# Kernel optimization log

Hardware: AMD Instinct MI355X
Metric: run time of the kernel (lower is better)

## Reference

```python
import jax, jax.numpy as jnp
import numpy as np

D = 1024      # d_model
H = 16        # num_heads
HW = D // H   # head_width = 64
FF = 4 * D    # hidden_dim = 4096
BATCH = 2
T = 2048
EPS = 1e-5


def layer_norm(x, g, b):
    mu = jnp.mean(x, axis=-1, keepdims=True)
    var = jnp.mean(jnp.square(x - mu), axis=-1, keepdims=True)
    return (x - mu) * jax.lax.rsqrt(var + EPS) * g + b


def setup_inputs() -> dict:
    key = jax.random.key(0)
    ks = jax.random.split(key, 7)
    s = 0.02
    return {
        "x": jax.random.normal(ks[0], (BATCH, T, D), dtype=jnp.float32),
        "Wq": jax.random.normal(ks[1], (D, D), dtype=jnp.float32) * s,
        "Wk": jax.random.normal(ks[2], (D, D), dtype=jnp.float32) * s,
        "Wv": jax.random.normal(ks[3], (D, D), dtype=jnp.float32) * s,
        "W1": jax.random.normal(ks[4], (FF, D), dtype=jnp.float32) * s,
        "W2": jax.random.normal(ks[5], (D, FF), dtype=jnp.float32) * s,
        "g1": jnp.ones((D,), dtype=jnp.float32),
        "b1": jnp.zeros((D,), dtype=jnp.float32),
        "g2": jnp.ones((D,), dtype=jnp.float32),
        "b2": jnp.zeros((D,), dtype=jnp.float32),
    }


def reference(x, Wq, Wk, Wv, W1, W2, g1, b1, g2, b2):
    N, t, d = x.shape
    # norm1
    xn = layer_norm(x, g1, b1)

    # --- MHSA with ALiBi + causal mask (math mirrors torch module) ---
    def heads(y):  # (N,t,D) -> (N,H,t,HW)
        return y.reshape(N, t, H, HW).transpose(0, 2, 1, 3)

    q = heads(xn @ Wq.T)
    k = heads(xn @ Wk.T)
    v = heads(xn @ Wv.T)

    scores = jnp.einsum("nhqd,nhkd->nhqk", q, k) / np.sqrt(HW).astype(np.float32)

    pos = jnp.arange(t)
    rel = (pos[None, :] - pos[:, None]).astype(x.dtype)           # [t,t], rel[i,j]=j-i
    slopes = (2.0 ** (-(jnp.arange(1, H + 1)) * (8.0 / H))).astype(x.dtype)  # [H]
    alibi = slopes[:, None, None] * rel                            # [H,t,t]
    causal = jnp.where(pos[None, :] > pos[:, None],
                       jnp.array(-jnp.inf, x.dtype),
                       jnp.array(0.0, x.dtype))                    # [t,t]

    att = jax.nn.softmax(scores + alibi[None] + causal[None, None], axis=-1)
    o = jnp.einsum("nhqk,nhkd->nhqd", att, v)
    o = o.transpose(0, 2, 1, 3).reshape(N, t, d)

    att_out = xn + o

    # --- MLP: Linear -> SiLU -> Linear ---
    h = layer_norm(att_out, g2, b2)
    m = jax.nn.silu(h @ W1.T) @ W2.T
    return att_out + m
```

## Files before the change

### kernel.cpp

```cpp
#include <hip/hip_runtime.h>

#define DMODEL 1024
#define NHEAD  16
#define HWID   64
#define FFDIM  4096
#define NBATCH 2
#define SEQT   2048
#define NTOK   4096
#define QKLD   3072

using bf8    = __attribute__((ext_vector_type(8))) short;
using f32x4  = __attribute__((ext_vector_type(4))) float;
using f32x16 = __attribute__((ext_vector_type(16))) float;

__device__ inline short to_bf16(float f) {
  unsigned u = __float_as_uint(f);
  return (short)((u + 0x7fffu + ((u >> 16) & 1u)) >> 16);
}
__device__ inline float from_bf16(short s) {
  return __uint_as_float(((unsigned)(unsigned short)s) << 16);
}
__device__ inline float exp2_fast(float x) {
  float r;
  asm("v_exp_f32 %0, %1" : "=v"(r) : "v"(x));
  return r;
}
__device__ inline unsigned cvt_pk_bf16(float lo, float hi) {
  unsigned r;
  asm("v_cvt_pk_bf16_f32 %0, %1, %2" : "=v"(r) : "v"(lo), "v"(hi));
  return r;
}
__device__ inline void lds_load16(const void* g, void* l) {
  __builtin_amdgcn_global_load_lds(
      (const __attribute__((address_space(1))) void*)g,
      (__attribute__((address_space(3))) void*)l, 16, 0, 0);
}

__global__ __launch_bounds__(256)
void cvt_all(const float* __restrict__ Wq, const float* __restrict__ Wk,
             const float* __restrict__ Wv, const float* __restrict__ W1,
             const float* __restrict__ W2, short* __restrict__ wqkv,
             short* __restrict__ w1b, short* __restrict__ w2b) {
  int i = blockIdx.x * 256 + threadIdx.x;
  const float* src;
  short* dst;
  if (i < 1048576)      { src = W1; dst = w1b; }
  else if (i < 2097152) { src = W2; dst = w2b;            i -= 1048576; }
  else if (i < 2359296) { src = Wq; dst = wqkv;           i -= 2097152; }
  else if (i < 2621440) { src = Wk; dst = wqkv + 1048576; i -= 2359296; }
  else                  { src = Wv; dst = wqkv + 2097152; i -= 2621440; }
  float4 v = ((const float4*)src)[i];
  short4 o;
  o.x = to_bf16(v.x); o.y = to_bf16(v.y);
  o.z = to_bf16(v.z); o.w = to_bf16(v.w);
  ((short4*)dst)[i] = o;
}

__global__ __launch_bounds__(256)
void ln_kernel(const float* __restrict__ x, const float* __restrict__ g,
               const float* __restrict__ b, short* __restrict__ out) {
  const int row = blockIdx.x;
  const int t = threadIdx.x;
  const float4 v = ((const float4*)(x + (long)row * DMODEL))[t];
  float s  = v.x + v.y + v.z + v.w;
  float s2 = v.x * v.x + v.y * v.y + v.z * v.z + v.w * v.w;
#pragma unroll
  for (int m = 1; m < 64; m <<= 1) {
    s  += __shfl_xor(s, m);
    s2 += __shfl_xor(s2, m);
  }
  __shared__ float red[8];
  if ((t & 63) == 0) { red[t >> 6] = s; red[4 + (t >> 6)] = s2; }
  __syncthreads();
  s  = red[0] + red[1] + red[2] + red[3];
  s2 = red[4] + red[5] + red[6] + red[7];
  const float mu = s * (1.f / DMODEL);
  const float rs = rsqrtf(s2 * (1.f / DMODEL) - mu * mu + 1e-5f);
  const float4 gv = ((const float4*)g)[t];
  const float4 bv = ((const float4*)b)[t];
  short4 o;
  o.x = to_bf16((v.x - mu) * rs * gv.x + bv.x);
  o.y = to_bf16((v.y - mu) * rs * gv.y + bv.y);
  o.z = to_bf16((v.z - mu) * rs * gv.z + bv.z);
  o.w = to_bf16((v.w - mu) * rs * gv.w + bv.w);
  ((short4*)(out + (long)row * DMODEL))[t] = o;
}

template <int EPI>
__global__ __launch_bounds__(256, 3)
void gemm4(const short* __restrict__ A, const short* __restrict__ Bw,
           void* __restrict__ Cout, int N, int lda, int ldb, int Kslice) {
  __shared__ short lds[3][2][4096];
  const int tid = threadIdx.x;
  const int w = tid >> 6, lane = tid & 63;
  const int l15 = lane & 15, l4 = lane >> 4;
  const int wr = (w >> 1) * 64, wc = (w & 1) * 64;

  const int gx = gridDim.x, nwg = gx * gridDim.y;
  const int wg = blockIdx.y * gx + blockIdx.x;
  const int sw = (wg & 7) * (nwg >> 3) + (wg >> 3);
  const int sx = gx >> 2;
  const int st = sw >> 4, w16 = sw & 15;
  const long bm = (long)((st / sx) * 4 + (w16 >> 2)) * 128;
  const long bn = (long)((st % sx) * 4 + (w16 & 3)) * 128;
  const long kofs = (long)blockIdx.z * Kslice;

  long aoff[2], boff[2];
#pragma unroll
  for (int i = 0; i < 2; ++i) {
    const int c = i * 4 + w;
    const int row = c * 16 + (lane >> 2);
    const int slog = (lane & 3) ^ ((row >> 1) & 3);
    aoff[i] = (bm + row) * (long)lda + slog * 8 + kofs;
    boff[i] = (bn + row) * (long)ldb + slog * 8 + kofs;
  }
  int offA[4], offB[4];
#pragma unroll
  for (int m = 0; m < 4; ++m) {
    const int row = wr + m * 16 + l15;
    offA[m] = row * 64 + ((l4 ^ ((row >> 1) & 3)) << 4);
  }
#pragma unroll
  for (int n = 0; n < 4; ++n) {
    const int row = wc + n * 16 + l15;
    offB[n] = row * 64 + ((l4 ^ ((row >> 1) & 3)) << 4);
  }

  const int NT = Kslice >> 5;
  f32x4 acc[4][4] = {};

#pragma unroll
  for (int t = 0; t < 2; ++t) {
    char* db = (char*)&lds[t][0][0];
#pragma unroll
    for (int i = 0; i < 2; ++i) {
      const int c = i * 4 + w;
      lds_load16(A  + aoff[i] + t * 32, db + c * 1024);
      lds_load16(Bw + boff[i] + t * 32, db + 8192 + c * 1024);
    }
  }

  int slot = 0, pslot = 2;
  for (int t = 0; t < NT; ++t) {
    if (t + 1 < NT) asm volatile("s_waitcnt vmcnt(4)" ::: "memory");
    else            asm volatile("s_waitcnt vmcnt(0)" ::: "memory");
    __builtin_amdgcn_s_barrier();
    asm volatile("" ::: "memory");
    if (t + 2 < NT) {
      char* db = (char*)&lds[pslot][0][0];
      const long ks = (long)(t + 2) * 32;
#pragma unroll
      for (int i = 0; i < 2; ++i) {
        const int c = i * 4 + w;
        lds_load16(A  + aoff[i] + ks, db + c * 1024);
        lds_load16(Bw + boff[i] + ks, db + 8192 + c * 1024);
      }
    }
    const char* sb = (const char*)&lds[slot][0][0];
    bf8 af[4], bfr[4];
#pragma unroll
    for (int m = 0; m < 4; ++m) af[m] = *(const bf8*)(sb + offA[m]);
#pragma unroll
    for (int n = 0; n < 4; ++n) bfr[n] = *(const bf8*)(sb + 8192 + offB[n]);
    __builtin_amdgcn_s_setprio(1);
#pragma unroll
    for (int m = 0; m < 4; ++m)
#pragma unroll
      for (int n = 0; n < 4; ++n)
        acc[m][n] = __builtin_amdgcn_mfma_f32_16x16x32_bf16(af[m], bfr[n], acc[m][n], 0, 0, 0);
    __builtin_amdgcn_s_setprio(0);
    slot  = (slot  == 2) ? 0 : slot  + 1;
    pslot = (pslot == 2) ? 0 : pslot + 1;
  }

#pragma unroll
  for (int m = 0; m < 4; ++m)
#pragma unroll
    for (int n = 0; n < 4; ++n) {
      const long col = bn + wc + n * 16 + l15;
#pragma unroll
      for (int r = 0; r < 4; ++r) {
        const long row = bm + wr + m * 16 + l4 * 4 + r;
        float v = acc[m][n][r];
        if (EPI == 0) {
          ((short*)Cout)[row * N + col] = to_bf16(v);
        } else if (EPI == 1) {
          ((short*)Cout)[row * N + col] = to_bf16(v / (1.f + __expf(-v)));
        } else {
          atomicAdd(&((float*)Cout)[row * N + col], v);
        }
      }
    }
}

__global__ __launch_bounds__(256)
void pack_kv(const short* __restrict__ qkv, short* __restrict__ Kp,
             short* __restrict__ Vp) {
  __shared__ short tile[64][72];
  const int bx = blockIdx.x, bh = blockIdx.y;
  const int b = bh >> 4, h = bh & 15;
  const int t = threadIdx.x;
  if (bx < 64) {
    const int g = bx;
    const int row = t >> 3, cc = t & 7, c = cc >> 1, hi = cc & 1;
    const bf8 v = *(const bf8*)&qkv[(long)(b * SEQT + g * 32 + row) * QKLD +
                                    1024 + h * HWID + c * 16 + hi * 8];
    *(bf8*)&Kp[(((long)bh * 256 + g * 4 + c) * 64 + hi * 32 + row) * 8] = v;
  } else {
    const int tc = bx - 64;
    {
      const int r = t >> 2, c = (t & 3) * 16;
      const long src = (long)(b * SEQT + tc * 64 + r) * QKLD + 2048 + h * HWID + c;
      *(bf8*)&tile[r][c]     = *(const bf8*)&qkv[src];
      *(bf8*)&tile[r][c + 8] = *(const bf8*)&qkv[src + 8];
    }
    __syncthreads();
    const int dg = t >> 7, ch = (t >> 5) & 3, row = t & 31;
#pragma unroll
    for (int hi = 0; hi < 2; ++hi) {
      short o[8];
#pragma unroll
      for (int j = 0; j < 8; ++j) o[j] = tile[ch * 16 + hi * 8 + j][dg * 32 + row];
      *(bf8*)&Vp[(((long)bh * 256 + dg * 128 + tc * 4 + ch) * 64 + hi * 32 + row) * 8] =
          *(bf8*)o;
    }
  }
}

__global__ __launch_bounds__(64, 2)
void attn_kernel(const short* __restrict__ qkv, const short* __restrict__ Kp,
                 const short* __restrict__ Vp, const short* __restrict__ xn,
                 float* __restrict__ att) {
  const int L = blockIdx.x;
  const int bh = (L & 7) * 4 + ((L >> 3) & 3);
  const int qtile = 63 - (L >> 5);
  const int b = bh >> 4, h = bh & 15;
  const int q0 = qtile * 32;
  const int lane = threadIdx.x;
  const int l31 = lane & 31, hi = lane >> 5;
  const long tokbase = (long)b * SEQT;

  bf8 qf[4];
  {
    const short* qrow = qkv + (tokbase + q0 + l31) * QKLD + h * HWID + hi * 8;
#pragma unroll
    for (int c = 0; c < 4; ++c) qf[c] = *(const bf8*)(qrow + c * 16);
  }

  const float slope2 = exp2f(-0.5f * (float)(h + 1)) * 1.44269504f;
  const float sc2 = 0.125f * 1.44269504f;
  float arr[16];
#pragma unroll
  for (int r = 0; r < 16; ++r) arr[r] = slope2 * (float)((r & 3) + 8 * (r >> 2));
  const float hofs = slope2 * 4.f * (float)hi;
  const float qabs = (float)(q0 + l31);

  float m2 = -1e30f, lsum = 0.f;
  f32x16 acc0 = {}, acc1 = {};
  const int ktm = q0 >> 6;
  const bf8* kfb = (const bf8*)Kp + (long)bh * 16384 + lane;
  const bf8* vfb = (const bf8*)Vp + (long)bh * 16384 + lane;

  bf8 kc[8], kn[8], vc[8];
#pragma unroll
  for (int c = 0; c < 4; ++c) {
    kc[c]     = kfb[c * 64];
    kc[4 + c] = kfb[256 + c * 64];
  }

#pragma unroll 2
  for (int kt = 0; kt <= ktm; ++kt) {
    const int k0 = kt * 64;
    const long vb = (long)kt * 256;
#pragma unroll
    for (int ch = 0; ch < 4; ++ch) {
      vc[ch]     = vfb[vb + ch * 64];
      vc[4 + ch] = vfb[8192 + vb + ch * 64];
    }
    const long nb = (long)(kt < ktm ? kt + 1 : kt) * 512;
#pragma unroll
    for (int c = 0; c < 4; ++c) {
      kn[c]     = kfb[nb + c * 64];
      kn[4 + c] = kfb[nb + 256 + c * 64];
    }
    f32x16 s0 = {}, s1 = {};
#pragma unroll
    for (int c = 0; c < 4; ++c) {
      s0 = __builtin_amdgcn_mfma_f32_32x32x16_bf16(kc[c], qf[c], s0, 0, 0, 0);
      s1 = __builtin_amdgcn_mfma_f32_32x32x16_bf16(kc[4 + c], qf[c], s1, 0, 0, 0);
    }
    const float base = slope2 * ((float)k0 - qabs) + hofs;
    float s[32];
#pragma unroll
    for (int r = 0; r < 16; ++r) {
      s[r]      = fmaf(s0[r], sc2, base + arr[r]);
      s[16 + r] = fmaf(s1[r], sc2, base + arr[r] + slope2 * 32.f);
    }
    if (kt == ktm) {
      const int qi = q0 + l31;
#pragma unroll
      for (int r = 0; r < 16; ++r) {
        const int krel = (r & 3) + 8 * (r >> 2) + 4 * hi;
        if (k0 + krel > qi)      s[r]      = -1e30f;
        if (k0 + 32 + krel > qi) s[16 + r] = -1e30f;
      }
    }
    float ma = s[0], mb = s[1], mc = s[2], md = s[3];
#pragma unroll
    for (int i = 4; i < 32; i += 4) {
      ma = fmaxf(ma, s[i]); mb = fmaxf(mb, s[i + 1]);
      mc = fmaxf(mc, s[i + 2]); md = fmaxf(md, s[i + 3]);
    }
    float pm = fmaxf(fmaxf(ma, mb), fmaxf(mc, md));
    pm = fmaxf(pm, __shfl_xor(pm, 32));
    if (!__all(pm - m2 <= 11.0f)) {
      const float nm = fmaxf(m2, pm);
      const float alpha = exp2_fast(m2 - nm);
      m2 = nm;
      lsum *= alpha;
      acc0 *= alpha;
      acc1 *= alpha;
    }
    float p[32];
#pragma unroll
    for (int i = 0; i < 32; ++i) p[i] = exp2_fast(s[i] - m2);
    float sa = p[0], sb = p[1], sc = p[2], sd = p[3];
#pragma unroll
    for (int i = 4; i < 32; i += 4) {
      sa += p[i]; sb += p[i + 1]; sc += p[i + 2]; sd += p[i + 3];
    }
    float rs = (sa + sb) + (sc + sd);
    rs += __shfl_xor(rs, 32);
    lsum += rs;
    unsigned cpk[16];
#pragma unroll
    for (int g = 0; g < 8; ++g) {
      cpk[g]     = cvt_pk_bf16(p[2 * g], p[2 * g + 1]);
      cpk[8 + g] = cvt_pk_bf16(p[16 + 2 * g], p[16 + 2 * g + 1]);
    }
    bf8 pb[4];
#pragma unroll
    for (int ch = 0; ch < 4; ++ch) {
      const int cb = (ch >> 1) * 8 + (ch & 1) * 4;
      unsigned u0 = cpk[cb + 0], u2 = cpk[cb + 2];
      unsigned u1 = cpk[cb + 1], u3 = cpk[cb + 3];
      asm("v_permlane32_swap_b32 %0, %1" : "+v"(u0), "+v"(u2));
      asm("v_permlane32_swap_b32 %0, %1" : "+v"(u1), "+v"(u3));
      union { unsigned u[4]; bf8 v; } f;
      f.u[0] = u0; f.u[1] = u1; f.u[2] = u2; f.u[3] = u3;
      pb[ch] = f.v;
    }
#pragma unroll
    for (int ch = 0; ch < 4; ++ch) {
      acc0 = __builtin_amdgcn_mfma_f32_32x32x16_bf16(vc[ch], pb[ch], acc0, 0, 0, 0);
      acc1 = __builtin_amdgcn_mfma_f32_32x32x16_bf16(vc[4 + ch], pb[ch], acc1, 0, 0, 0);
    }
#pragma unroll
    for (int i = 0; i < 8; ++i) kc[i] = kn[i];
  }

  __shared__ float Os[32 * 68];
  const float rl = 1.f / lsum;
#pragma unroll
  for (int r = 0; r < 16; ++r) {
    const int d0 = (r & 3) + 8 * (r >> 2) + 4 * hi;
    Os[l31 * 68 + d0]      = acc0[r] * rl;
    Os[l31 * 68 + 32 + d0] = acc1[r] * rl;
  }
  __syncthreads();
#pragma unroll
  for (int it = 0; it < 8; ++it) {
    const int idx = it * 64 + lane;
    const int row = idx >> 4, c4 = idx & 15;
    const float4 ov = *(const float4*)&Os[row * 68 + c4 * 4];
    const long gbase = (tokbase + q0 + row) * DMODEL + h * HWID + c4 * 4;
    const short4 xv = *(const short4*)&xn[gbase];
    float4 o;
    o.x = ov.x + from_bf16(xv.x);
    o.y = ov.y + from_bf16(xv.y);
    o.z = ov.z + from_bf16(xv.z);
    o.w = ov.w + from_bf16(xv.w);
    *(float4*)&att[gbase] = o;
  }
}

extern "C" void kernel_launch(void* const* d_in, const int* in_sizes, int n_in,
                              void* d_out, int out_size, void* d_ws, size_t ws_size,
                              hipStream_t stream) {
  (void)in_sizes; (void)n_in; (void)out_size; (void)ws_size;
  const float* x  = (const float*)d_in[0];
  const float* Wq = (const float*)d_in[1];
  const float* Wk = (const float*)d_in[2];
  const float* Wv = (const float*)d_in[3];
  const float* W1 = (const float*)d_in[4];
  const float* W2 = (const float*)d_in[5];
  const float* g1 = (const float*)d_in[6];
  const float* b1 = (const float*)d_in[7];
  const float* g2 = (const float*)d_in[8];
  const float* b2 = (const float*)d_in[9];

  char* ws = (char*)d_ws;
  const size_t MB = 1024 * 1024;
  short* wqkv_b = (short*)(ws + 0);
  short* w1_b   = (short*)(ws + 6  * MB);
  short* w2_b   = (short*)(ws + 14 * MB);
  short* xn     = (short*)(ws + 22 * MB);
  short* qkv    = (short*)(ws + 30 * MB);
  short* m1     = (short*)(ws + 22 * MB);
  short* Kp     = (short*)(ws + 54 * MB);
  short* Vp     = (short*)(ws + 62 * MB);
  short* hb     = (short*)(ws + 70 * MB);
  float* att    = (float*)d_out;

  cvt_all<<<11264, 256, 0, stream>>>(Wq, Wk, Wv, W1, W2, wqkv_b, w1_b, w2_b);

  ln_kernel<<<NTOK, 256, 0, stream>>>(x, g1, b1, xn);

  gemm4<0><<<dim3(24, 32), 256, 0, stream>>>(xn, wqkv_b, qkv, QKLD, DMODEL, DMODEL, DMODEL);
  pack_kv<<<dim3(96, 32), 256, 0, stream>>>(qkv, Kp, Vp);

  attn_kernel<<<2048, 64, 0, stream>>>(qkv, Kp, Vp, xn, att);

  ln_kernel<<<NTOK, 256, 0, stream>>>(att, g2, b2, hb);

  gemm4<1><<<dim3(32, 32), 256, 0, stream>>>(hb, w1_b, m1, FFDIM, DMODEL, DMODEL, DMODEL);
  gemm4<3><<<dim3(8, 32, 4), 256, 0, stream>>>(m1, w2_b, d_out, DMODEL, FFDIM, FFDIM, 1024);
}
```

Measured before the change: 232.2 us.

## Enlarge GEMM tile to 256x128 and replace split-K atomics with partial buffers

Doubles the GEMM block tile along M to 256 rows, so each wave computes 8x4 MFMA fragments and every B tile loaded into LDS is reused across more rows. Grids and occupancy hints are halved to match. The split-K down-projection now writes per-slice partial results to a workspace buffer instead of issuing float atomics. A new combine kernel sums the partials into the output. This trades more registers and LDS per block, plus an extra pass over about 64MB of partials, for higher arithmetic intensity and no atomic contention.

```diff
diff --git a/kernel.cpp b/kernel.cpp
--- a/kernel.cpp
+++ b/kernel.cpp
@@ -87,84 +87,91 @@
 }
 
 template <int EPI>
-__global__ __launch_bounds__(256, 3)
+__global__ __launch_bounds__(256, 2)
 void gemm4(const short* __restrict__ A, const short* __restrict__ Bw,
-           void* __restrict__ Cout, int N, int lda, int ldb, int Kslice) {
-  __shared__ short lds[3][2][4096];
+           void* __restrict__ Cout, int N, int lda, int ldb, int Kslice,
+           long zstride) {
+  __shared__ short lds[3][12288];
   const int tid = threadIdx.x;
   const int w = tid >> 6, lane = tid & 63;
   const int l15 = lane & 15, l4 = lane >> 4;
-  const int wr = (w >> 1) * 64, wc = (w & 1) * 64;
+  const int wm = w >> 1, wn = w & 1;
 
   const int gx = gridDim.x, nwg = gx * gridDim.y;
   const int wg = blockIdx.y * gx + blockIdx.x;
   const int sw = (wg & 7) * (nwg >> 3) + (wg >> 3);
   const int sx = gx >> 2;
   const int st = sw >> 4, w16 = sw & 15;
-  const long bm = (long)((st / sx) * 4 + (w16 >> 2)) * 128;
+  const long bm = (long)((st / sx) * 4 + (w16 >> 2)) * 256;
   const long bn = (long)((st % sx) * 4 + (w16 & 3)) * 128;
   const long kofs = (long)blockIdx.z * Kslice;
 
-  long aoff[2], boff[2];
+  long aoff[4], boff[2];
+#pragma unroll
+  for (int i = 0; i < 4; ++i) {
+    const int c = i * 4 + w;
+    const int row = c * 16 + (lane >> 2);
+    const int slog = (lane & 3) ^ ((row >> 1) & 3);
+    aoff[i] = (bm + row) * (long)lda + slog * 8 + kofs;
+  }
 #pragma unroll
   for (int i = 0; i < 2; ++i) {
     const int c = i * 4 + w;
     const int row = c * 16 + (lane >> 2);
     const int slog = (lane & 3) ^ ((row >> 1) & 3);
-    aoff[i] = (bm + row) * (long)lda + slog * 8 + kofs;
     boff[i] = (bn + row) * (long)ldb + slog * 8 + kofs;
   }
-  int offA[4], offB[4];
-#pragma unroll
-  for (int m = 0; m < 4; ++m) {
-    const int row = wr + m * 16 + l15;
+  int offA[8], offB[4];
+#pragma unroll
+  for (int m = 0; m < 8; ++m) {
+    const int row = wm * 128 + m * 16 + l15;
     offA[m] = row * 64 + ((l4 ^ ((row >> 1) & 3)) << 4);
   }
 #pragma unroll
   for (int n = 0; n < 4; ++n) {
-    const int row = wc + n * 16 + l15;
+    const int row = wn * 64 + n * 16 + l15;
     offB[n] = row * 64 + ((l4 ^ ((row >> 1) & 3)) << 4);
   }
 
   const int NT = Kslice >> 5;
-  f32x4 acc[4][4] = {};
+  f32x4 acc[8][4] = {};
 
 #pragma unroll
   for (int t = 0; t < 2; ++t) {
-    char* db = (char*)&lds[t][0][0];
-#pragma unroll
-    for (int i = 0; i < 2; ++i) {
-      const int c = i * 4 + w;
-      lds_load16(A  + aoff[i] + t * 32, db + c * 1024);
-      lds_load16(Bw + boff[i] + t * 32, db + 8192 + c * 1024);
-    }
+    char* db = (char*)&lds[t][0];
+#pragma unroll
+    for (int i = 0; i < 4; ++i)
+      lds_load16(A + aoff[i] + t * 32, db + (i * 4 + w) * 1024);
+#pragma unroll
+    for (int i = 0; i < 2; ++i)
+      lds_load16(Bw + boff[i] + t * 32, db + 16384 + (i * 4 + w) * 1024);
   }
 
   int slot = 0, pslot = 2;
   for (int t = 0; t < NT; ++t) {
-    if (t + 1 < NT) asm volatile("s_waitcnt vmcnt(4)" ::: "memory");
+    if (t + 1 < NT) asm volatile("s_waitcnt vmcnt(6)" ::: "memory");
     else            asm volatile("s_waitcnt vmcnt(0)" ::: "memory");
     __builtin_amdgcn_s_barrier();
     asm volatile("" ::: "memory");
     if (t + 2 < NT) {
-      char* db = (char*)&lds[pslot][0][0];
+      char* db = (char*)&lds[pslot][0];
       const long ks = (long)(t + 2) * 32;
 #pragma unroll
-      for (int i = 0; i < 2; ++i) {
-        const int c = i * 4 + w;
-        lds_load16(A  + aoff[i] + ks, db + c * 1024);
-        lds_load16(Bw + boff[i] + ks, db + 8192 + c * 1024);
-      }
-    }
-    const char* sb = (const char*)&lds[slot][0][0];
-    bf8 af[4], bfr[4];
-#pragma unroll
-    for (int m = 0; m < 4; ++m) af[m] = *(const bf8*)(sb + offA[m]);
-#pragma unroll
-    for (int n = 0; n < 4; ++n) bfr[n] = *(const bf8*)(sb + 8192 + offB[n]);
+      for (int i = 0; i < 4; ++i)
+        lds_load16(A + aoff[i] + ks, db + (i * 4 + w) * 1024);
+#pragma unroll
+      for (int i = 0; i < 2; ++i)
+        lds_load16(Bw + boff[i] + ks, db + 16384 + (i * 4 + w) * 1024);
+    }
+    const char* sb = (const char*)&lds[slot][0];
+    bf8 af[8], bfr[4];
+#pragma unroll
+    for (int m = 0; m < 8; ++m) af[m] = *(const bf8*)(sb + offA[m]);
+#pragma unroll
+    for (int n = 0; n < 4; ++n) bfr[n] = *(const bf8*)(sb + 16384 + offB[n]);
     __builtin_amdgcn_s_setprio(1);
 #pragma unroll
-    for (int m = 0; m < 4; ++m)
+    for (int m = 0; m < 8; ++m)
 #pragma unroll
       for (int n = 0; n < 4; ++n)
         acc[m][n] = __builtin_amdgcn_mfma_f32_16x16x32_bf16(af[m], bfr[n], acc[m][n], 0, 0, 0);
@@ -173,21 +180,22 @@
     pslot = (pslot == 2) ? 0 : pslot + 1;
   }
 
-#pragma unroll
-  for (int m = 0; m < 4; ++m)
+  float* Cp = (float*)Cout + (EPI == 2 ? (long)blockIdx.z * zstride : 0);
+#pragma unroll
+  for (int m = 0; m < 8; ++m)
 #pragma unroll
     for (int n = 0; n < 4; ++n) {
-      const long col = bn + wc + n * 16 + l15;
+      const long col = bn + wn * 64 + n * 16 + l15;
 #pragma unroll
       for (int r = 0; r < 4; ++r) {
-        const long row = bm + wr + m * 16 + l4 * 4 + r;
+        const long row = bm + wm * 128 + m * 16 + l4 * 4 + r;
         float v = acc[m][n][r];
         if (EPI == 0) {
           ((short*)Cout)[row * N + col] = to_bf16(v);
         } else if (EPI == 1) {
           ((short*)Cout)[row * N + col] = to_bf16(v / (1.f + __expf(-v)));
         } else {
-          atomicAdd(&((float*)Cout)[row * N + col], v);
+          Cp[row * N + col] = v;
         }
       }
     }
@@ -384,6 +392,23 @@
   }
 }
 
+__global__ __launch_bounds__(256)
+void combine_kernel(const float* __restrict__ p, float* __restrict__ dout, int n4) {
+  int i = blockIdx.x * 256 + threadIdx.x;
+  if (i < n4) {
+    float4 a  = ((const float4*)dout)[i];
+    float4 b0 = ((const float4*)(p))[i];
+    float4 b1 = ((const float4*)(p + 4194304))[i];
+    float4 b2 = ((const float4*)(p + 8388608))[i];
+    float4 b3 = ((const float4*)(p + 12582912))[i];
+    a.x += (b0.x + b1.x) + (b2.x + b3.x);
+    a.y += (b0.y + b1.y) + (b2.y + b3.y);
+    a.z += (b0.z + b1.z) + (b2.z + b3.z);
+    a.w += (b0.w + b1.w) + (b2.w + b3.w);
+    ((float4*)dout)[i] = a;
+  }
+}
+
 extern "C" void kernel_launch(void* const* d_in, const int* in_sizes, int n_in,
                               void* d_out, int out_size, void* d_ws, size_t ws_size,
                               hipStream_t stream) {
@@ -410,19 +435,24 @@
   short* Kp     = (short*)(ws + 54 * MB);
   short* Vp     = (short*)(ws + 62 * MB);
   short* hb     = (short*)(ws + 70 * MB);
+  float* parts  = (float*)(ws + 54 * MB);
   float* att    = (float*)d_out;
 
   cvt_all<<<11264, 256, 0, stream>>>(Wq, Wk, Wv, W1, W2, wqkv_b, w1_b, w2_b);
 
   ln_kernel<<<NTOK, 256, 0, stream>>>(x, g1, b1, xn);
 
-  gemm4<0><<<dim3(24, 32), 256, 0, stream>>>(xn, wqkv_b, qkv, QKLD, DMODEL, DMODEL, DMODEL);
+  gemm4<0><<<dim3(24, 16), 256, 0, stream>>>(xn, wqkv_b, qkv, QKLD, DMODEL, DMODEL,
+                                             DMODEL, 0);
   pack_kv<<<dim3(96, 32), 256, 0, stream>>>(qkv, Kp, Vp);
 
   attn_kernel<<<2048, 64, 0, stream>>>(qkv, Kp, Vp, xn, att);
 
   ln_kernel<<<NTOK, 256, 0, stream>>>(att, g2, b2, hb);
 
-  gemm4<1><<<dim3(32, 32), 256, 0, stream>>>(hb, w1_b, m1, FFDIM, DMODEL, DMODEL, DMODEL);
-  gemm4<3><<<dim3(8, 32, 4), 256, 0, stream>>>(m1, w2_b, d_out, DMODEL, FFDIM, FFDIM, 1024);
-}
+  gemm4<1><<<dim3(32, 16), 256, 0, stream>>>(hb, w1_b, m1, FFDIM, DMODEL, DMODEL,
+                                             DMODEL, 0);
+  gemm4<2><<<dim3(8, 16, 4), 256, 0, stream>>>(m1, w2_b, parts, DMODEL, FFDIM, FFDIM,
+                                               1024, (long)NTOK * DMODEL);
+  combine_kernel<<<4096, 256, 0, stream>>>(parts, (float*)d_out, 1048576);
+}
```

New measurement: 205.0 us. 11.7% less time.
